# Optimization experiments

Measured on AMD Instinct MI355X. Metric: run time of the kernel, lower is better.

## Reference

```python
import jax, jax.numpy as jnp
import numpy as np
from jax import lax

EPS = 1e-5
DW_THR = 4.0    # threshold for depthwise-branch channel pruning
PW_THR = 0.001  # threshold for pointwise-branch channel pruning


def _bn(x, gamma, beta, mean, var):
    # inference-mode BatchNorm2d over channel dim (NCHW)
    inv = gamma / jnp.sqrt(var + EPS)
    return x * inv[None, :, None, None] + (beta - mean * inv)[None, :, None, None]


def _prune(x, thr):
    # zero every (batch, channel) slice whose max abs value is < thr
    keep = jnp.max(jnp.abs(x), axis=(2, 3), keepdims=True) >= thr  # [B,C,1,1]
    return x * lax.stop_gradient(keep).astype(x.dtype)


def setup_inputs() -> dict:
    key = jax.random.key(0)
    ks = jax.random.split(key, 12)
    B, C, O, H, W = 64, 128, 256, 56, 56
    x = jax.random.normal(ks[0], (B, C, H, W), jnp.float32)
    dw_w = jax.random.normal(ks[1], (C, 1, 3, 3), jnp.float32) * 0.2   # depthwise OIHW, groups=C
    dw_b = jax.random.normal(ks[2], (C,), jnp.float32) * 0.1
    g1 = 1.0 + 0.2 * jax.random.normal(ks[3], (C,), jnp.float32)
    b1 = 0.1 * jax.random.normal(ks[4], (C,), jnp.float32)
    m1 = 0.1 * jax.random.normal(ks[5], (C,), jnp.float32)
    v1 = jax.random.uniform(ks[6], (C,), jnp.float32, 0.5, 1.5)
    pw_w = jax.random.normal(ks[7], (O, C, 1, 1), jnp.float32) * (1.0 / np.sqrt(C))
    pw_b = jax.random.normal(ks[8], (O,), jnp.float32) * 0.1
    g2 = 1.0 + 0.2 * jax.random.normal(ks[9], (O,), jnp.float32)
    b2 = 0.1 * jax.random.normal(ks[10], (O,), jnp.float32)
    m2 = 0.1 * jax.random.normal(ks[11], (O,), jnp.float32)
    v2 = jnp.ones((O,), jnp.float32)
    return {"x": x, "dw_w": dw_w, "dw_b": dw_b, "g1": g1, "b1": b1, "m1": m1, "v1": v1,
            "pw_w": pw_w, "pw_b": pw_b, "g2": g2, "b2": b2, "m2": m2, "v2": v2}


def reference(x, dw_w, dw_b, g1, b1, m1, v1, pw_w, pw_b, g2, b2, m2, v2):
    C = dw_w.shape[0]
    # depthwise 3x3 conv, padding=1, groups=C
    y = lax.conv_general_dilated(
        x, dw_w, window_strides=(1, 1), padding=[(1, 1), (1, 1)],
        dimension_numbers=("NCHW", "OIHW", "NCHW"), feature_group_count=C)
    y = y + dw_b[None, :, None, None]
    y = jax.nn.relu(_bn(y, g1, b1, m1, v1))
    y = _prune(y, DW_THR)
    # pointwise 1x1 conv
    z = jnp.einsum("bchw,oc->bohw", y, pw_w[:, :, 0, 0]) + pw_b[None, :, None, None]
    z = jax.nn.relu(_bn(z, g2, b2, m2, v2))
    z = _prune(z, PW_THR)
    return z
```

## Files before the change

kernel.cpp:

```cpp
#include <hip/hip_runtime.h>
#include <stdint.h>

#define EPSV 1e-5f

typedef __attribute__((ext_vector_type(8))) short short8;
typedef __attribute__((ext_vector_type(4))) float floatx4;

__device__ __forceinline__ unsigned short f2bf(float f) {
    union { float f; uint32_t u; } v; v.f = f;
    uint32_t u = v.u;
    return (unsigned short)((u + 0x7FFFu + ((u >> 16) & 1u)) >> 16);
}

__global__ __launch_bounds__(256) void k_dw(
        const float* __restrict__ x, const float* __restrict__ dw_w,
        const float* __restrict__ dw_b, const float* __restrict__ g1,
        const float* __restrict__ b1, const float* __restrict__ m1,
        const float* __restrict__ v1,
        const float* __restrict__ pw_w, const float* __restrict__ pw_b,
        const float* __restrict__ g2, const float* __restrict__ b2,
        const float* __restrict__ m2, const float* __restrict__ v2,
        unsigned short* __restrict__ y_ws,
        unsigned short* __restrict__ w_bf, float* __restrict__ bias2) {
    const int c = blockIdx.x, b = blockIdx.y;
    const int t = threadIdx.x;
    __shared__ float halo[58 * 58];
    __shared__ float red[4];

    if (b == 0) {
        int idx = c * 256 + t;
        int o = idx >> 7, cc = idx & 127;
        float inv = g2[o] / sqrtf(v2[o] + EPSV);
        w_bf[idx] = f2bf(pw_w[idx] * inv);
        if (cc == 0) bias2[o] = pw_b[o] * inv + b2[o] - m2[o] * inv;
    }

    const float* xs = x + (size_t)(b * 128 + c) * 3136;
    if (t < 228) {
        int pos;
        if (t < 58)       pos = t;
        else if (t < 116) pos = 57 * 58 + (t - 58);
        else if (t < 172) pos = (t - 115) * 58;
        else              pos = (t - 171) * 58 + 57;
        halo[pos] = 0.f;
    }
    {
        const floatx4* x4 = (const floatx4*)xs;
        #pragma unroll
        for (int i = 0; i < 4; ++i) {
            int f = t + 256 * i;
            if (f < 784) {
                floatx4 v = x4[f];
                int p = 4 * f;
                int h = p / 56, ww = p - h * 56;
                float* d = &halo[(h + 1) * 58 + ww + 1];
                d[0] = v[0]; d[1] = v[1]; d[2] = v[2]; d[3] = v[3];
            }
        }
    }
    const float* wk = dw_w + c * 9;
    float k0 = wk[0], k1 = wk[1], k2 = wk[2], k3 = wk[3], k4 = wk[4],
          k5 = wk[5], k6 = wk[6], k7 = wk[7], k8 = wk[8];
    float inv1 = g1[c] / sqrtf(v1[c] + EPSV);
    float add0 = dw_b[c] * inv1 + b1[c] - m1[c] * inv1;
    __syncthreads();

    float yv[14];
    float mx = 0.f;
    #pragma unroll
    for (int i = 0; i < 7; ++i) {
        int base = i * 512 + 2 * t;
        if (base < 3136) {
            int h = base / 56, w = base - h * 56;
            const float* r0 = &halo[h * 58 + w];
            const float* r1 = r0 + 58;
            const float* r2 = r1 + 58;
            float a0 = r0[0], a1 = r0[1], a2 = r0[2], a3 = r0[3];
            float b0 = r1[0], b1_ = r1[1], b2_ = r1[2], b3 = r1[3];
            float c0 = r2[0], c1 = r2[1], c2 = r2[2], c3 = r2[3];
            float s0 = k0*a0 + k1*a1 + k2*a2 + k3*b0 + k4*b1_ + k5*b2_ + k6*c0 + k7*c1 + k8*c2;
            float s1 = k0*a1 + k1*a2 + k2*a3 + k3*b1_ + k4*b2_ + k5*b3 + k6*c1 + k7*c2 + k8*c3;
            float y0 = fmaxf(s0 * inv1 + add0, 0.f);
            float y1 = fmaxf(s1 * inv1 + add0, 0.f);
            mx = fmaxf(mx, fmaxf(y0, y1));
            yv[2 * i] = y0; yv[2 * i + 1] = y1;
        }
    }
    #pragma unroll
    for (int off = 32; off; off >>= 1) mx = fmaxf(mx, __shfl_xor(mx, off));
    if ((t & 63) == 0) red[t >> 6] = mx;
    __syncthreads();
    float m4 = fmaxf(fmaxf(red[0], red[1]), fmaxf(red[2], red[3]));
    float scale = (m4 >= 4.0f) ? 1.f : 0.f;

    uint32_t* yo = (uint32_t*)(y_ws + (size_t)(b * 128 + c) * 3136);
    #pragma unroll
    for (int i = 0; i < 7; ++i) {
        int base = i * 512 + 2 * t;
        if (base < 3136) {
            unsigned short h0 = f2bf(yv[2 * i] * scale);
            unsigned short h1 = f2bf(yv[2 * i + 1] * scale);
            yo[base >> 1] = (uint32_t)h0 | ((uint32_t)h1 << 16);
        }
    }
}

__global__ __launch_bounds__(256, 2) void k_pw(
        const unsigned short* __restrict__ y,
        const unsigned short* __restrict__ w_bf,
        const float* __restrict__ bias2, float* __restrict__ z) {
    const int nt = blockIdx.x;
    const int b  = blockIdx.y;
    const int t = threadIdx.x;
    const int w = t >> 6, lane = t & 63;
    const int q = lane >> 4, r = lane & 15;
    __shared__ __align__(16) char smem[33792];
    short* B_s = (short*)smem;
    float* E   = (float*)smem;

    short8 a[4][4];
    #pragma unroll
    for (int it = 0; it < 4; ++it)
        #pragma unroll
        for (int kk = 0; kk < 4; ++kk)
            a[it][kk] = *(const short8*)(w_bf +
                (size_t)(w * 64 + it * 16 + r) * 128 + kk * 32 + q * 8);

    {
        const int n0 = nt * 128;
        const int nch = (t & 15) * 8;
        const int sw = (t & 7) << 4;
        #pragma unroll
        for (int i = 0; i < 8; ++i) {
            int c = (t >> 4) + i * 16;
            int cp = c ^ sw;
            uint4 v = make_uint4(0, 0, 0, 0);
            if (n0 + nch < 3136)
                v = *(const uint4*)(y + (size_t)(b * 128 + c) * 3136 + n0 + nch);
            const short* sv = (const short*)&v;
            #pragma unroll
            for (int j = 0; j < 8; ++j)
                B_s[(nch + j) * 128 + cp] = sv[j];
        }
    }
    __syncthreads();

    floatx4 acc[4][8];
    #pragma unroll
    for (int i = 0; i < 4; ++i)
        #pragma unroll
        for (int j = 0; j < 8; ++j) acc[i][j] = (floatx4)0.f;

    #pragma unroll
    for (int kk = 0; kk < 4; ++kk) {
        short8 bb[8];
        #pragma unroll
        for (int jt = 0; jt < 8; ++jt) {
            int nl = jt * 16 + r;
            int cs = (kk * 32 + q * 8) ^ ((((nl >> 3) & 7)) << 4);
            bb[jt] = *(const short8*)&B_s[nl * 128 + cs];
        }
        #pragma unroll
        for (int it = 0; it < 4; ++it)
            #pragma unroll
            for (int jt = 0; jt < 8; ++jt)
                acc[it][jt] = __builtin_amdgcn_mfma_f32_16x16x32_bf16(
                    a[it][kk], bb[jt], acc[it][jt], 0, 0, 0);
    }

    const int n_base = nt * 128;
    float* zb = z + (size_t)b * 256 * 3136;
    #pragma unroll
    for (int it = 0; it < 4; ++it) {
        int o0 = w * 64 + it * 16 + q * 4;
        floatx4 bias = *(const floatx4*)(bias2 + o0);
        __syncthreads();
        #pragma unroll
        for (int jt = 0; jt < 8; ++jt) {
            int n = jt * 16 + r;
            #pragma unroll
            for (int j = 0; j < 4; ++j)
                E[(w * 16 + q * 4 + j) * 132 + n] =
                    fmaxf(acc[it][jt][j] + bias[j], 0.f);
        }
        __syncthreads();
        #pragma unroll
        for (int s = 0; s < 8; ++s) {
            int idx = t + 256 * s;
            int rho = idx >> 5, n4 = (idx & 31) * 4;
            if (n_base + n4 < 3136) {
                floatx4 v = *(const floatx4*)&E[rho * 132 + n4];
                int o = (rho >> 4) * 64 + it * 16 + (rho & 15);
                __builtin_nontemporal_store(v,
                    (floatx4*)(zb + (size_t)o * 3136 + n_base + n4));
            }
        }
    }
}

extern "C" void kernel_launch(void* const* d_in, const int* in_sizes, int n_in,
                              void* d_out, int out_size, void* d_ws, size_t ws_size,
                              hipStream_t stream) {
    const float* x    = (const float*)d_in[0];
    const float* dw_w = (const float*)d_in[1];
    const float* dw_b = (const float*)d_in[2];
    const float* g1   = (const float*)d_in[3];
    const float* b1   = (const float*)d_in[4];
    const float* m1   = (const float*)d_in[5];
    const float* v1   = (const float*)d_in[6];
    const float* pw_w = (const float*)d_in[7];
    const float* pw_b = (const float*)d_in[8];
    const float* g2   = (const float*)d_in[9];
    const float* b2   = (const float*)d_in[10];
    const float* m2   = (const float*)d_in[11];
    const float* v2   = (const float*)d_in[12];
    float* z = (float*)d_out;

    const size_t YB = 51380224;
    unsigned short* y_ws = (unsigned short*)d_ws;
    unsigned short* w_bf = (unsigned short*)((char*)d_ws + YB);
    float* bias2         = (float*)((char*)d_ws + YB + 65536);

    hipLaunchKernelGGL(k_dw, dim3(128, 64), dim3(256), 0, stream,
                       x, dw_w, dw_b, g1, b1, m1, v1,
                       pw_w, pw_b, g2, b2, m2, v2, y_ws, w_bf, bias2);
    hipLaunchKernelGGL(k_pw, dim3(25, 64), dim3(256), 0, stream,
                       y_ws, w_bf, bias2, z);
}
```

Baseline: 331.4 us.

## Vectorize depthwise halo/stencil, repack pointwise B tile, use per-warp epilogue staging

The depthwise kernel now uses a 60-wide, 16-byte-aligned halo so it can do vector LDS stores and loads, and computes 8 outputs per thread with a single 16-byte bf16 store. The pointwise kernel permutes the weight K order in the prep step so that the B tile can be transposed in registers and written to LDS with 16-byte stores into a padded, XOR-swizzled layout, replacing scalar short stores. The epilogue gives each wave its own staging region, which removes the block-wide barriers per output tile at the cost of more LDS. The goal is fewer LDS instructions and bank conflicts; the risks are higher register pressure and subtle correctness issues from the index permutation.

```diff
diff --git a/kernel.cpp b/kernel.cpp
--- a/kernel.cpp
+++ b/kernel.cpp
@@ -5,6 +5,7 @@
 
 typedef __attribute__((ext_vector_type(8))) short short8;
 typedef __attribute__((ext_vector_type(4))) float floatx4;
+typedef __attribute__((ext_vector_type(2))) float float2v;
 
 __device__ __forceinline__ unsigned short f2bf(float f) {
     union { float f; uint32_t u; } v; v.f = f;
@@ -24,25 +25,27 @@
         unsigned short* __restrict__ w_bf, float* __restrict__ bias2) {
     const int c = blockIdx.x, b = blockIdx.y;
     const int t = threadIdx.x;
-    __shared__ float halo[58 * 58];
+    __shared__ __align__(16) float halo_buf[4 + 58 * 60];
     __shared__ float red[4];
+    float* halo = halo_buf + 4;
 
     if (b == 0) {
         int idx = c * 256 + t;
-        int o = idx >> 7, cc = idx & 127;
+        int o = idx >> 7, s = idx & 127;
+        int csrc = ((s >> 5) << 2) + ((s >> 3) & 3) + ((s & 7) << 4);
         float inv = g2[o] / sqrtf(v2[o] + EPSV);
-        w_bf[idx] = f2bf(pw_w[idx] * inv);
-        if (cc == 0) bias2[o] = pw_b[o] * inv + b2[o] - m2[o] * inv;
+        w_bf[idx] = f2bf(pw_w[o * 128 + csrc] * inv);
+        if (s == 0) bias2[o] = pw_b[o] * inv + b2[o] - m2[o] * inv;
     }
 
     const float* xs = x + (size_t)(b * 128 + c) * 3136;
-    if (t < 228) {
-        int pos;
-        if (t < 58)       pos = t;
-        else if (t < 116) pos = 57 * 58 + (t - 58);
-        else if (t < 172) pos = (t - 115) * 58;
-        else              pos = (t - 171) * 58 + 57;
-        halo[pos] = 0.f;
+
+    {
+        floatx4 zz = {0.f, 0.f, 0.f, 0.f};
+        if (t < 15)       *(floatx4*)(halo + 4 * t) = zz;
+        else if (t < 30)  *(floatx4*)(halo + 57 * 60 + 4 * (t - 15)) = zz;
+        else if (t < 86)  *(floatx4*)(halo + (t - 29) * 60 + 56) = zz;
+        else if (t == 86) *(floatx4*)halo_buf = zz;
     }
     {
         const floatx4* x4 = (const floatx4*)xs;
@@ -53,8 +56,7 @@
                 floatx4 v = x4[f];
                 int p = 4 * f;
                 int h = p / 56, ww = p - h * 56;
-                float* d = &halo[(h + 1) * 58 + ww + 1];
-                d[0] = v[0]; d[1] = v[1]; d[2] = v[2]; d[3] = v[3];
+                *(floatx4*)(halo + (h + 1) * 60 + ww) = v;
             }
         }
     }
@@ -65,25 +67,37 @@
     float add0 = dw_b[c] * inv1 + b1[c] - m1[c] * inv1;
     __syncthreads();
 
-    float yv[14];
+    float yv[16];
     float mx = 0.f;
     #pragma unroll
-    for (int i = 0; i < 7; ++i) {
-        int base = i * 512 + 2 * t;
-        if (base < 3136) {
-            int h = base / 56, w = base - h * 56;
-            const float* r0 = &halo[h * 58 + w];
-            const float* r1 = r0 + 58;
-            const float* r2 = r1 + 58;
-            float a0 = r0[0], a1 = r0[1], a2 = r0[2], a3 = r0[3];
-            float b0 = r1[0], b1_ = r1[1], b2_ = r1[2], b3 = r1[3];
-            float c0 = r2[0], c1 = r2[1], c2 = r2[2], c3 = r2[3];
-            float s0 = k0*a0 + k1*a1 + k2*a2 + k3*b0 + k4*b1_ + k5*b2_ + k6*c0 + k7*c1 + k8*c2;
-            float s1 = k0*a1 + k1*a2 + k2*a3 + k3*b1_ + k4*b2_ + k5*b3 + k6*c1 + k7*c2 + k8*c3;
-            float y0 = fmaxf(s0 * inv1 + add0, 0.f);
-            float y1 = fmaxf(s1 * inv1 + add0, 0.f);
-            mx = fmaxf(mx, fmaxf(y0, y1));
-            yv[2 * i] = y0; yv[2 * i + 1] = y1;
+    for (int gi = 0; gi < 2; ++gi) {
+        int g = t + gi * 256;
+        if (g < 392) {
+            int gh = g / 7, gw = (g - gh * 7) * 8;
+            const float* p0 = halo + gh * 60 + gw;
+            float w0[10], w1[10], w2[10];
+#define LOADROW(dst, p) { \
+            float2v L_ = *(const float2v*)((p) - 2); \
+            floatx4 M0_ = *(const floatx4*)(p); \
+            floatx4 M1_ = *(const floatx4*)((p) + 4); \
+            float2v R_ = *(const float2v*)((p) + 8); \
+            dst[0] = L_[1]; \
+            dst[1] = M0_[0]; dst[2] = M0_[1]; dst[3] = M0_[2]; dst[4] = M0_[3]; \
+            dst[5] = M1_[0]; dst[6] = M1_[1]; dst[7] = M1_[2]; dst[8] = M1_[3]; \
+            dst[9] = R_[0]; }
+            LOADROW(w0, p0)
+            LOADROW(w1, p0 + 60)
+            LOADROW(w2, p0 + 120)
+#undef LOADROW
+            #pragma unroll
+            for (int j = 0; j < 8; ++j) {
+                float s = k0 * w0[j] + k1 * w0[j + 1] + k2 * w0[j + 2]
+                        + k3 * w1[j] + k4 * w1[j + 1] + k5 * w1[j + 2]
+                        + k6 * w2[j] + k7 * w2[j + 1] + k8 * w2[j + 2];
+                float yy = fmaxf(s * inv1 + add0, 0.f);
+                mx = fmaxf(mx, yy);
+                yv[gi * 8 + j] = yy;
+            }
         }
     }
     #pragma unroll
@@ -93,14 +107,21 @@
     float m4 = fmaxf(fmaxf(red[0], red[1]), fmaxf(red[2], red[3]));
     float scale = (m4 >= 4.0f) ? 1.f : 0.f;
 
-    uint32_t* yo = (uint32_t*)(y_ws + (size_t)(b * 128 + c) * 3136);
-    #pragma unroll
-    for (int i = 0; i < 7; ++i) {
-        int base = i * 512 + 2 * t;
-        if (base < 3136) {
-            unsigned short h0 = f2bf(yv[2 * i] * scale);
-            unsigned short h1 = f2bf(yv[2 * i + 1] * scale);
-            yo[base >> 1] = (uint32_t)h0 | ((uint32_t)h1 << 16);
+    unsigned short* yo = y_ws + (size_t)(b * 128 + c) * 3136;
+    #pragma unroll
+    for (int gi = 0; gi < 2; ++gi) {
+        int g = t + gi * 256;
+        if (g < 392) {
+            uint4 pkv;
+            uint32_t pk[4];
+            #pragma unroll
+            for (int j2 = 0; j2 < 4; ++j2) {
+                unsigned short h0 = f2bf(yv[gi * 8 + 2 * j2] * scale);
+                unsigned short h1 = f2bf(yv[gi * 8 + 2 * j2 + 1] * scale);
+                pk[j2] = (uint32_t)h0 | ((uint32_t)h1 << 16);
+            }
+            pkv.x = pk[0]; pkv.y = pk[1]; pkv.z = pk[2]; pkv.w = pk[3];
+            *(uint4*)(yo + g * 8) = pkv;
         }
     }
 }
@@ -114,9 +135,8 @@
     const int t = threadIdx.x;
     const int w = t >> 6, lane = t & 63;
     const int q = lane >> 4, r = lane & 15;
-    __shared__ __align__(16) char smem[33792];
+    __shared__ __align__(16) char smem[36864];
     short* B_s = (short*)smem;
-    float* E   = (float*)smem;
 
     short8 a[4][4];
     #pragma unroll
@@ -127,20 +147,31 @@
                 (size_t)(w * 64 + it * 16 + r) * 128 + kk * 32 + q * 8);
 
     {
-        const int n0 = nt * 128;
-        const int nch = (t & 15) * 8;
-        const int sw = (t & 7) << 4;
+        const int n0g = nt * 128;
+        const int nb = (t & 15) * 8;
+        const bool valid = (n0g + nb < 3136);
+        uint32_t Vd[8][4];
+        const unsigned short* yb = y + (size_t)(b * 128) * 3136 + n0g + nb;
         #pragma unroll
         for (int i = 0; i < 8; ++i) {
-            int c = (t >> 4) + i * 16;
-            int cp = c ^ sw;
-            uint4 v = make_uint4(0, 0, 0, 0);
-            if (n0 + nch < 3136)
-                v = *(const uint4*)(y + (size_t)(b * 128 + c) * 3136 + n0 + nch);
-            const short* sv = (const short*)&v;
-            #pragma unroll
-            for (int j = 0; j < 8; ++j)
-                B_s[(nch + j) * 128 + cp] = sv[j];
+            int cc = (t >> 4) + i * 16;
+            uint4 v = make_uint4(0u, 0u, 0u, 0u);
+            if (valid) v = *(const uint4*)(yb + (size_t)cc * 3136);
+            Vd[i][0] = v.x; Vd[i][1] = v.y; Vd[i][2] = v.z; Vd[i][3] = v.w;
+        }
+        const int slot_w = (t >> 4) ^ (t & 15);
+        #pragma unroll
+        for (int j = 0; j < 8; ++j) {
+            const int sh = (j & 1) * 16;
+            uint32_t Wd[4];
+            #pragma unroll
+            for (int k2 = 0; k2 < 4; ++k2) {
+                uint32_t lo = (Vd[2 * k2][j >> 1] >> sh) & 0xffffu;
+                uint32_t hi = (Vd[2 * k2 + 1][j >> 1] >> sh) & 0xffffu;
+                Wd[k2] = lo | (hi << 16);
+            }
+            uint4 wv; wv.x = Wd[0]; wv.y = Wd[1]; wv.z = Wd[2]; wv.w = Wd[3];
+            *(uint4*)&B_s[(nb + j) * 144 + slot_w * 8] = wv;
         }
     }
     __syncthreads();
@@ -157,8 +188,8 @@
         #pragma unroll
         for (int jt = 0; jt < 8; ++jt) {
             int nl = jt * 16 + r;
-            int cs = (kk * 32 + q * 8) ^ ((((nl >> 3) & 7)) << 4);
-            bb[jt] = *(const short8*)&B_s[nl * 128 + cs];
+            int slot_r = (kk * 4 + q) ^ (nl >> 3);
+            bb[jt] = *(const short8*)&B_s[nl * 144 + slot_r * 8];
         }
         #pragma unroll
         for (int it = 0; it < 4; ++it)
@@ -168,29 +199,30 @@
                     a[it][kk], bb[jt], acc[it][jt], 0, 0, 0);
     }
 
+    __syncthreads();
+    float* Ew = (float*)smem + w * 2112;
     const int n_base = nt * 128;
     float* zb = z + (size_t)b * 256 * 3136;
     #pragma unroll
     for (int it = 0; it < 4; ++it) {
         int o0 = w * 64 + it * 16 + q * 4;
         floatx4 bias = *(const floatx4*)(bias2 + o0);
-        __syncthreads();
         #pragma unroll
         for (int jt = 0; jt < 8; ++jt) {
             int n = jt * 16 + r;
             #pragma unroll
             for (int j = 0; j < 4; ++j)
-                E[(w * 16 + q * 4 + j) * 132 + n] =
-                    fmaxf(acc[it][jt][j] + bias[j], 0.f);
-        }
-        __syncthreads();
+                Ew[(q * 4 + j) * 132 + n] = fmaxf(acc[it][jt][j] + bias[j], 0.f);
+        }
+        asm volatile("s_waitcnt lgkmcnt(0)" ::: "memory");
+        __builtin_amdgcn_sched_barrier(0);
         #pragma unroll
         for (int s = 0; s < 8; ++s) {
-            int idx = t + 256 * s;
-            int rho = idx >> 5, n4 = (idx & 31) * 4;
+            int chunk = s * 64 + lane;
+            int rho = chunk >> 5, n4 = (chunk & 31) * 4;
             if (n_base + n4 < 3136) {
-                floatx4 v = *(const floatx4*)&E[rho * 132 + n4];
-                int o = (rho >> 4) * 64 + it * 16 + (rho & 15);
+                floatx4 v = *(const floatx4*)&Ew[rho * 132 + n4];
+                int o = w * 64 + it * 16 + rho;
                 __builtin_nontemporal_store(v,
                     (floatx4*)(zb + (size_t)o * 3136 + n_base + n4));
             }
```

Result: faster. 322.9 us (-2.6%).
